# Optimization experiments

Hardware: AMD Instinct MI355X
Metric: run time of the kernel (lower is better)

## Reference

```python
import jax, jax.numpy as jnp
import numpy as np

B, T, C = 2, 2048, 1024
NHEADS = 16
HEAD_DIM = C // NHEADS  # 64
THETA = 10000.0
SCALE_BASE = 512.0
GN_EPS = 1e-5


def setup_inputs() -> dict:
    key = jax.random.key(0)
    ks = jax.random.split(key, 4)
    s = 0.02
    return {
        "x": jax.random.normal(ks[0], (B, T, C), jnp.float32),
        "w_qkv": jax.random.normal(ks[1], (3 * C, C), jnp.float32) * s,
        "w_gated": jax.random.normal(ks[2], (C, C), jnp.float32) * s,
        "w_proj": jax.random.normal(ks[3], (C, C), jnp.float32) * s,
        "gn_weight": jnp.ones((C,), jnp.float32),
        "gn_bias": jnp.zeros((C,), jnp.float32),
    }


def _rotate_half(x):
    # pairs are adjacent/interleaved: (d r) with r=2
    x1 = x[..., 0::2]
    x2 = x[..., 1::2]
    return jnp.stack([-x2, x1], axis=-1).reshape(x.shape)


def _rope_xpos(q, k, T):
    # lucidrains rotary_embedding_torch with use_xpos=True
    d = q.shape[-1]
    half = jnp.arange(0, d, 2, dtype=jnp.float32)
    inv_freq = 1.0 / (THETA ** (half / d))
    t = jnp.arange(T, dtype=jnp.float32)
    freqs = t[:, None] * inv_freq[None, :]          # [T, d/2]
    freqs = jnp.repeat(freqs, 2, axis=-1)           # [T, d] interleaved
    scale_vec = (half + 0.4 * d) / (1.4 * d)        # [d/2]
    power = (t - T // 2) / SCALE_BASE               # [T]
    scale = scale_vec[None, :] ** power[:, None]    # [T, d/2]
    scale = jnp.repeat(scale, 2, axis=-1)           # [T, d]
    cos, sin = jnp.cos(freqs), jnp.sin(freqs)
    q = q * (cos * scale) + _rotate_half(q) * (sin * scale)
    k = k * (cos / scale) + _rotate_half(k) * (sin / scale)
    return q, k


def _decay_mask(T):
    # gamma_h = 1 - 2^(-5-h); mask[h,i,j] = gamma_h^(i-j) for i>=j else 0
    gamma = 1.0 - 2.0 ** (-5.0 - jnp.arange(NHEADS, dtype=jnp.float32))
    idx = jnp.arange(T)
    diff = idx[:, None] - idx[None, :]              # [T, T]
    causal = diff >= 0
    expn = jnp.where(causal, diff, 0).astype(jnp.float32)
    return jnp.where(causal[None], gamma[:, None, None] ** expn[None], 0.0)


def reference(x, w_qkv, w_gated, w_proj, gn_weight, gn_bias):
    Bx, Tx, Cx = x.shape
    qkv = x @ w_qkv.T                               # [B,T,3C]
    q, k, v = jnp.split(qkv, 3, axis=-1)
    def to_heads(u):
        return u.reshape(Bx, Tx, NHEADS, HEAD_DIM).transpose(0, 2, 1, 3)
    q, k, v = to_heads(q), to_heads(k), to_heads(v)  # [B,H,T,D]
    q, k = _rope_xpos(q, k, Tx)
    mask = _decay_mask(Tx)                           # [H,T,T]
    scores = jnp.einsum('bhtd,bhsd->bhts', q, k) * (HEAD_DIM ** -0.5)
    scores = scores * mask[None]
    y = jnp.einsum('bhts,bhsd->bhtd', scores, v)     # [B,H,T,D]
    y = y.transpose(0, 2, 1, 3).reshape(Bx, Tx, Cx)  # [B,T,C]
    # GroupNorm over (B, C, T) with num_groups = NHEADS: normalize each
    # group's (C/H channels x T positions) jointly.
    yt = y.transpose(0, 2, 1).reshape(Bx, NHEADS, HEAD_DIM, Tx)
    mean = yt.mean(axis=(2, 3), keepdims=True)
    var = yt.var(axis=(2, 3), keepdims=True)
    yn = (yt - mean) / jnp.sqrt(var + GN_EPS)
    yn = yn.reshape(Bx, Cx, Tx)
    yn = yn * gn_weight[None, :, None] + gn_bias[None, :, None]
    yn = yn.transpose(0, 2, 1)                       # [B,T,C]
    out = jax.nn.silu(x @ w_gated.T) * yn
    return out @ w_proj.T
```

## Files before the change

kernel.cpp:

```cpp
#include <hip/hip_runtime.h>

typedef __attribute__((ext_vector_type(8))) short bf16x8;
typedef __attribute__((ext_vector_type(4))) float f32x4;
typedef __attribute__((ext_vector_type(16))) float f32x16;
typedef __attribute__((ext_vector_type(2))) unsigned short u16x2;
typedef __attribute__((ext_vector_type(4))) unsigned short u16x4;
typedef __attribute__((ext_vector_type(2))) unsigned int u32x2;

static constexpr int kB = 2;
static constexpr int kT = 2048;
static constexpr int kC = 1024;
static constexpr int kH = 16;
static constexpr int kD = 64;
static constexpr int kNC = 16;

__device__ inline unsigned short f2bf(float f) {
    unsigned int u = __float_as_uint(f);
    u += 0x7FFFu + ((u >> 16) & 1u);
    return (unsigned short)(u >> 16);
}
__device__ inline float bf2f(unsigned short u) {
    return __uint_as_float(((unsigned int)u) << 16);
}

#define GLDS16(g, s)                                                            \
    __builtin_amdgcn_global_load_lds(                                           \
        (const __attribute__((address_space(1))) unsigned int*)(g),             \
        (__attribute__((address_space(3))) unsigned int*)(s), 16, 0, 0)

__global__ __launch_bounds__(256) void cvt_bf16(const float* __restrict__ in,
                                                unsigned short* __restrict__ out, int n) {
    int i = (blockIdx.x * 256 + threadIdx.x) * 4;
    if (i >= n) return;
    float4 v = *(const float4*)(in + i);
    u16x4 o;
    o[0] = f2bf(v.x); o[1] = f2bf(v.y); o[2] = f2bf(v.z); o[3] = f2bf(v.w);
    *(u16x4*)(out + i) = o;
}

__global__ __launch_bounds__(256) void make_tables(float2* __restrict__ qtab,
                                                   float2* __restrict__ ktab,
                                                   float* __restrict__ decq,
                                                   float* __restrict__ deck) {
    int idx = blockIdx.x * 256 + threadIdx.x;
    if (idx < kT * 32) {
        int t = idx >> 5, i = idx & 31;
        float half = 2.0f * (float)i;
        float inv_freq = powf(10000.0f, -half / 64.0f);
        float fr = (float)t * inv_freq;
        float sv = (half + 0.4f * 64.0f) / (1.4f * 64.0f);
        float p = ((float)t - 1024.0f) / 512.0f;
        float scl = powf(sv, p);
        float c = cosf(fr), s = sinf(fr);
        qtab[idx] = make_float2(c * scl, s * scl);
        ktab[idx] = make_float2(c / scl, s / scl);
    }
    if (idx < kH * 128) {
        int h = idx >> 7, tt = idx & 127;
        float log2g = log2f(1.0f - exp2f(-5.0f - (float)h));
        decq[idx] = 0.125f * exp2f(log2g * (float)tt);
        deck[idx] = exp2f(-log2g * (float)tt);
    }
}

__global__ __launch_bounds__(256) void gemm_qkvg(const unsigned short* __restrict__ A,
                                                 const unsigned short* __restrict__ Bm,
                                                 unsigned short* __restrict__ qb,
                                                 unsigned short* __restrict__ kbuf,
                                                 unsigned short* __restrict__ vtb,
                                                 unsigned short* __restrict__ gbuf) {
    constexpr int K = 1024;
    __shared__ __align__(16) unsigned short Al[128 * 64];
    __shared__ __align__(16) unsigned short Bl[128 * 64];
    char* ab = (char*)Al;
    char* bb = (char*)Bl;
    const int tid = threadIdx.x;
    const int l = tid & 63, w = tid >> 6;
    const int wr = w >> 1, wc = w & 1;
    const int tm = blockIdx.y * 128, tn = blockIdx.x * 128;
    const int ri = l >> 3;
    const int su = (l & 7) ^ (ri & 7);

    f32x4 zero4 = {0.0f, 0.0f, 0.0f, 0.0f};
    f32x4 acc[4][4];
#pragma unroll
    for (int m = 0; m < 4; m++)
#pragma unroll
        for (int n = 0; n < 4; n++) acc[m][n] = zero4;

    for (int kt = 0; kt < K; kt += 64) {
#pragma unroll
        for (int c = w; c < 32; c += 4) {
            if (c < 16) {
                const unsigned short* src = A + (size_t)(tm + c * 8 + ri) * K + kt + su * 8;
                GLDS16(src, ab + c * 1024);
            } else {
                int cb = c - 16;
                const unsigned short* src = Bm + (size_t)(tn + cb * 8 + ri) * K + kt + su * 8;
                GLDS16(src, bb + cb * 1024);
            }
        }
        __syncthreads();
#pragma unroll
        for (int ks = 0; ks < 2; ks++) {
            bf16x8 af[4], bfr[4];
            int kbyte = ks * 64 + (l >> 4) * 16;
#pragma unroll
            for (int m = 0; m < 4; m++) {
                int row = wr * 64 + m * 16 + (l & 15);
                af[m] = *(const bf16x8*)(ab + row * 128 + (kbyte ^ ((row & 7) << 4)));
            }
#pragma unroll
            for (int n = 0; n < 4; n++) {
                int row = wc * 64 + n * 16 + (l & 15);
                bfr[n] = *(const bf16x8*)(bb + row * 128 + (kbyte ^ ((row & 7) << 4)));
            }
#pragma unroll
            for (int m = 0; m < 4; m++)
#pragma unroll
                for (int n = 0; n < 4; n++)
                    acc[m][n] = __builtin_amdgcn_mfma_f32_16x16x32_bf16(af[m], bfr[n], acc[m][n], 0, 0, 0);
        }
        __syncthreads();
    }

    if (tn < 2048) {
        const bool isq = (tn < 1024);
        unsigned short* dst = isq ? qb : kbuf;
        const int colbase = isq ? tn : (tn - 1024);
#pragma unroll
        for (int n = 0; n < 4; n++) {
            int col = colbase + wc * 64 + n * 16 + (l & 15);
            int h = col >> 6;
            int d = col & 63;
#pragma unroll
            for (int m = 0; m < 4; m++) {
#pragma unroll
                for (int r = 0; r < 4; r++) {
                    int row = tm + wr * 64 + m * 16 + (l >> 4) * 4 + r;
                    int b = row >> 11, t = row & 2047;
                    unsigned int ub = f2bf(acc[m][n][r]);
                    unsigned int pb = (unsigned int)__shfl_xor((int)ub, 1);
                    if (!(l & 1)) {
                        unsigned int packed = (ub & 0xFFFFu) | (pb << 16);
                        *(unsigned int*)(dst + ((size_t)(b * 16 + h) * 2048 + t) * 64 + d) = packed;
                    }
                }
            }
        }
    } else if (tn < 3072) {
#pragma unroll
        for (int m = 0; m < 4; m++)
#pragma unroll
            for (int n = 0; n < 4; n++) {
                int col2 = (tn - 2048) + wc * 64 + n * 16 + (l & 15);
                int rowb = tm + wr * 64 + m * 16 + (l >> 4) * 4;
                int b = rowb >> 11, t = rowb & 2047;
                u16x4 o;
#pragma unroll
                for (int r = 0; r < 4; r++) o[r] = f2bf(acc[m][n][r]);
                *(u16x4*)(vtb + ((size_t)(b * 1024 + col2)) * 2048 + t) = o;
            }
    } else {
#pragma unroll
        for (int n = 0; n < 4; n++) {
            int col3 = (tn - 3072) + wc * 64 + n * 16 + (l & 15);
#pragma unroll
            for (int m = 0; m < 4; m++) {
#pragma unroll
                for (int r = 0; r < 4; r++) {
                    int row = tm + wr * 64 + m * 16 + (l >> 4) * 4 + r;
                    float v = acc[m][n][r];
                    float sv2 = v / (1.0f + expf(-v));
                    unsigned int ub = f2bf(sv2);
                    unsigned int pb = (unsigned int)__shfl_xor((int)ub, 1);
                    if (!(l & 1)) {
                        unsigned int packed = (ub & 0xFFFFu) | (pb << 16);
                        *(unsigned int*)(gbuf + (size_t)row * 1024 + col3) = packed;
                    }
                }
            }
        }
    }
}

__global__ __launch_bounds__(256) void rope_qkt(unsigned short* __restrict__ qb,
                                                unsigned short* __restrict__ kbuf,
                                                unsigned short* __restrict__ ktb,
                                                const float2* __restrict__ qtab,
                                                const float2* __restrict__ ktab,
                                                const float* __restrict__ decq,
                                                const float* __restrict__ deck) {
    __shared__ unsigned short tile[64][72];
    const int bh = blockIdx.x;
    const int tt = blockIdx.y * 64;
    const int h = bh & 15;
    const int tl = threadIdx.x >> 2;
    const int du = (threadIdx.x & 3) * 16;
    const int t = tt + tl;
    const float dq = decq[h * 128 + (t & 127)];
    const float dk = deck[h * 128 + (t & 127)];

    {
        unsigned short* qrow = qb + ((size_t)bh * kT + t) * kD + du;
        bf16x8 a0 = *(const bf16x8*)(qrow);
        bf16x8 a1 = *(const bf16x8*)(qrow + 8);
        bf16x8 o0, o1;
#pragma unroll
        for (int j = 0; j < 4; ++j) {
            float2 cs = qtab[t * 32 + (du >> 1) + j];
            float x0 = bf2f((unsigned short)a0[2 * j]);
            float x1 = bf2f((unsigned short)a0[2 * j + 1]);
            o0[2 * j] = (short)f2bf((x0 * cs.x - x1 * cs.y) * dq);
            o0[2 * j + 1] = (short)f2bf((x1 * cs.x + x0 * cs.y) * dq);
            float2 cs2 = qtab[t * 32 + (du >> 1) + 4 + j];
            float y0 = bf2f((unsigned short)a1[2 * j]);
            float y1 = bf2f((unsigned short)a1[2 * j + 1]);
            o1[2 * j] = (short)f2bf((y0 * cs2.x - y1 * cs2.y) * dq);
            o1[2 * j + 1] = (short)f2bf((y1 * cs2.x + y0 * cs2.y) * dq);
        }
        *(bf16x8*)(qrow) = o0;
        *(bf16x8*)(qrow + 8) = o1;
    }
    {
        unsigned short* krow = kbuf + ((size_t)bh * kT + t) * kD + du;
        bf16x8 a0 = *(const bf16x8*)(krow);
        bf16x8 a1 = *(const bf16x8*)(krow + 8);
        bf16x8 o0, o1;
#pragma unroll
        for (int j = 0; j < 4; ++j) {
            float2 cs = ktab[t * 32 + (du >> 1) + j];
            float x0 = bf2f((unsigned short)a0[2 * j]);
            float x1 = bf2f((unsigned short)a0[2 * j + 1]);
            o0[2 * j] = (short)f2bf((x0 * cs.x - x1 * cs.y) * dk);
            o0[2 * j + 1] = (short)f2bf((x1 * cs.x + x0 * cs.y) * dk);
            float2 cs2 = ktab[t * 32 + (du >> 1) + 4 + j];
            float y0 = bf2f((unsigned short)a1[2 * j]);
            float y1 = bf2f((unsigned short)a1[2 * j + 1]);
            o1[2 * j] = (short)f2bf((y0 * cs2.x - y1 * cs2.y) * dk);
            o1[2 * j + 1] = (short)f2bf((y1 * cs2.x + y0 * cs2.y) * dk);
        }
        *(bf16x8*)(krow) = o0;
        *(bf16x8*)(krow + 8) = o1;
#pragma unroll
        for (int e = 0; e < 8; ++e) {
            tile[tl][du + e] = (unsigned short)o0[e];
            tile[tl][du + 8 + e] = (unsigned short)o1[e];
        }
    }
    __syncthreads();
    {
        int dd = threadIdx.x >> 2;
        int tb2 = (threadIdx.x & 3) * 16;
        bf16x8 o0, o1;
#pragma unroll
        for (int e = 0; e < 8; ++e) {
            o0[e] = (short)tile[tb2 + e][dd];
            o1[e] = (short)tile[tb2 + 8 + e][dd];
        }
        unsigned short* drow = ktb + ((size_t)bh * kD + dd) * kT + tt + tb2;
        *(bf16x8*)(drow) = o0;
        *(bf16x8*)(drow + 8) = o1;
    }
}

__global__ __launch_bounds__(256) void chunk_m(const unsigned short* __restrict__ ktb,
                                               const unsigned short* __restrict__ vtb,
                                               unsigned short* __restrict__ Mt) {
    __shared__ __align__(16) unsigned short Ktl[64 * 128];
    __shared__ __align__(16) unsigned short Vtl[64 * 128];
    const int tid = threadIdx.x, l = tid & 63, w = tid >> 6;
    const int bh = blockIdx.x, c = blockIdx.y, h = bh & 15;
    const int ql = l & 31, hi5 = l >> 5;
    char* kp = (char*)Ktl;
    char* vp = (char*)Vtl;
#pragma unroll
    for (int j = 0; j < 4; ++j) {
        int ch = w * 4 + j;
        int row = ch * 4 + (l >> 4);
        int u = (l & 15) ^ (row & 15);
        GLDS16(ktb + ((size_t)bh * kD + row) * kT + c * 128 + u * 8, kp + ch * 1024);
        GLDS16(vtb + ((size_t)bh * kD + row) * kT + c * 128 + u * 8, vp + ch * 1024);
    }
    __syncthreads();
    const int iw = w >> 1, jw = w & 1;
    f32x16 acc;
#pragma unroll
    for (int r = 0; r < 16; ++r) acc[r] = 0.0f;
#pragma unroll
    for (int sk = 0; sk < 8; ++sk) {
        int rowa = iw * 32 + ql;
        int rowb = jw * 32 + ql;
        bf16x8 av = *(const bf16x8*)(vp + rowa * 256 + 16 * ((2 * sk + hi5) ^ (rowa & 15)));
        bf16x8 bk = *(const bf16x8*)(kp + rowb * 256 + 16 * ((2 * sk + hi5) ^ (rowb & 15)));
        acc = __builtin_amdgcn_mfma_f32_32x32x16_bf16(av, bk, acc, 0, 0, 0);
    }
    float log2g = log2f(1.0f - exp2f(-5.0f - (float)h));
    float gC = exp2f(128.0f * log2g);
    unsigned short* mo = Mt + ((size_t)(bh * kNC + c)) * 4096;
#pragma unroll
    for (int r = 0; r < 16; ++r) {
        int row = iw * 32 + (r & 3) + 8 * (r >> 2) + 4 * hi5;
        int col = jw * 32 + ql;
        mo[row * 64 + col] = f2bf(acc[r] * gC);
    }
}

__global__ __launch_bounds__(256) void chunk_states(const unsigned short* __restrict__ Mt,
                                                    unsigned short* __restrict__ St) {
    const int bh = blockIdx.x, h = bh & 15;
    const int tid = threadIdx.x;
    float log2g = log2f(1.0f - exp2f(-5.0f - (float)h));
    float gC = exp2f(128.0f * log2g);
    float state[16];
#pragma unroll
    for (int e = 0; e < 16; ++e) state[e] = 0.0f;
    for (int c = 0; c < kNC; ++c) {
        unsigned short* so = St + ((size_t)(bh * kNC + c)) * 4096;
        const unsigned short* m = Mt + ((size_t)(bh * kNC + c)) * 4096;
#pragma unroll
        for (int k = 0; k < 4; ++k) {
            u16x4 o;
#pragma unroll
            for (int e = 0; e < 4; ++e) o[e] = f2bf(state[k * 4 + e]);
            *(u16x4*)(so + (k * 256 + tid) * 4) = o;
            u16x4 v = *(const u16x4*)(m + (k * 256 + tid) * 4);
#pragma unroll
            for (int e = 0; e < 4; ++e)
                state[k * 4 + e] = state[k * 4 + e] * gC + bf2f(v[e]);
        }
    }
}

__global__ __launch_bounds__(512) void chunk_attn(const unsigned short* __restrict__ qb,
                                                  const unsigned short* __restrict__ kb,
                                                  const unsigned short* __restrict__ vtb,
                                                  const unsigned short* __restrict__ St,
                                                  unsigned short* __restrict__ yb,
                                                  float* __restrict__ part) {
    __shared__ __align__(16) unsigned short Kt[128 * 64];
    __shared__ __align__(16) unsigned short Vt[64 * 128];
    __shared__ __align__(16) unsigned short Ss[64 * 64];
    __shared__ __align__(16) unsigned short Pl[8 * 32 * 64];
    __shared__ float red[16];
    const int tid = threadIdx.x, l = tid & 63, w = tid >> 6;
    const int bh = blockIdx.x, c = blockIdx.y;
    const int qw = w >> 1, dw = w & 1;
    const int ql = l & 31, hi5 = l >> 5;
    char* kp = (char*)Kt;
    char* vp = (char*)Vt;
    char* sp = (char*)Ss;
    char* pw = (char*)Pl + w * 4096;

#pragma unroll
    for (int j = 0; j < 2; ++j) {
        int ch = w * 2 + j;
        int row = ch * 8 + (l >> 3);
        int u = (l & 7) ^ (row & 7);
        GLDS16(kb + ((size_t)bh * kT + c * 128 + row) * kD + u * 8, kp + ch * 1024);
    }
#pragma unroll
    for (int j = 0; j < 2; ++j) {
        int ch = w * 2 + j;
        int row = ch * 4 + (l >> 4);
        int u = (l & 15) ^ (row & 15);
        GLDS16(vtb + ((size_t)bh * kD + row) * kT + c * 128 + u * 8, vp + ch * 1024);
    }
    {
        int row = w * 8 + (l >> 3);
        int u = (l & 7) ^ (row & 7);
        GLDS16(St + ((size_t)(bh * kNC + c)) * 4096 + row * 64 + u * 8, sp + w * 1024);
    }
    bf16x8 aq[4];
    {
        const unsigned short* qrow = qb + ((size_t)bh * kT + c * 128 + qw * 32 + ql) * kD + hi5 * 8;
#pragma unroll
        for (int dk = 0; dk < 4; ++dk) aq[dk] = *(const bf16x8*)(qrow + dk * 16);
    }
    __syncthreads();

    f32x16 acc;
#pragma unroll
    for (int r = 0; r < 16; ++r) acc[r] = 0.0f;
    const int qidx = qw * 32 + ql;

#pragma unroll
    for (int p = 0; p < 2; ++p) {
        f32x16 sA, sB;
#pragma unroll
        for (int r = 0; r < 16; ++r) { sA[r] = 0.0f; sB[r] = 0.0f; }
#pragma unroll
        for (int dk = 0; dk < 4; ++dk) {
            int rowa = (2 * p) * 32 + ql;
            int rowb = (2 * p + 1) * 32 + ql;
            bf16x8 ka = *(const bf16x8*)(kp + rowa * 128 + 16 * ((2 * dk + hi5) ^ (rowa & 7)));
            bf16x8 kb2 = *(const bf16x8*)(kp + rowb * 128 + 16 * ((2 * dk + hi5) ^ (rowb & 7)));
            sA = __builtin_amdgcn_mfma_f32_32x32x16_bf16(ka, aq[dk], sA, 0, 0, 0);
            sB = __builtin_amdgcn_mfma_f32_32x32x16_bf16(kb2, aq[dk], sB, 0, 0, 0);
        }
#pragma unroll
        for (int sb2 = 0; sb2 < 2; ++sb2) {
            int sbase = (2 * p + sb2) * 32 + 4 * hi5;
#pragma unroll
            for (int m = 0; m < 4; ++m) {
                float v0, v1, v2, v3;
                {
                    int s0i = sbase + 8 * m;
                    float x0 = sb2 ? sB[4 * m + 0] : sA[4 * m + 0];
                    float x1 = sb2 ? sB[4 * m + 1] : sA[4 * m + 1];
                    float x2 = sb2 ? sB[4 * m + 2] : sA[4 * m + 2];
                    float x3 = sb2 ? sB[4 * m + 3] : sA[4 * m + 3];
                    v0 = (qidx >= s0i + 0) ? x0 : 0.0f;
                    v1 = (qidx >= s0i + 1) ? x1 : 0.0f;
                    v2 = (qidx >= s0i + 2) ? x2 : 0.0f;
                    v3 = (qidx >= s0i + 3) ? x3 : 0.0f;
                }
                unsigned int lo, hi;
                asm("v_cvt_pk_bf16_f32 %0, %1, %2" : "=v"(lo) : "v"(v0), "v"(v1));
                asm("v_cvt_pk_bf16_f32 %0, %1, %2" : "=v"(hi) : "v"(v2), "v"(v3));
                u32x2 pr; pr[0] = lo; pr[1] = hi;
                *(u32x2*)(pw + ql * 128 + (((sb2 * 4 + m) * 16) ^ ((ql & 7) << 4)) + hi5 * 8) = pr;
            }
        }
#pragma unroll
        for (int kki = 0; kki < 4; ++kki) {
            bf16x8 ap = *(const bf16x8*)(pw + ql * 128 + 16 * ((2 * kki + hi5) ^ (ql & 7)));
            int rowv = dw * 32 + ql;
            bf16x8 bv = *(const bf16x8*)(vp + rowv * 256 + 16 * ((2 * (4 * p + kki) + hi5) ^ (rowv & 15)));
            acc = __builtin_amdgcn_mfma_f32_32x32x16_bf16(ap, bv, acc, 0, 0, 0);
        }
    }
#pragma unroll
    for (int dk = 0; dk < 4; ++dk) {
        int rows = dw * 32 + ql;
        bf16x8 bs = *(const bf16x8*)(sp + rows * 128 + 16 * ((2 * dk + hi5) ^ (rows & 7)));
        acc = __builtin_amdgcn_mfma_f32_32x32x16_bf16(aq[dk], bs, acc, 0, 0, 0);
    }
    float s = 0.0f, s2 = 0.0f;
#pragma unroll
    for (int r = 0; r < 16; ++r) {
        int row = c * 128 + qw * 32 + (r & 3) + 8 * (r >> 2) + 4 * hi5;
        int col = dw * 32 + ql;
        unsigned short ub = f2bf(acc[r]);
        yb[((size_t)bh * kT + row) * kD + col] = ub;
        float f = bf2f(ub);
        s += f; s2 += f * f;
    }
#pragma unroll
    for (int o = 32; o > 0; o >>= 1) {
        s += __shfl_down(s, o);
        s2 += __shfl_down(s2, o);
    }
    if (l == 0) { red[w * 2] = s; red[w * 2 + 1] = s2; }
    __syncthreads();
    if (tid == 0) {
        float S = 0.0f, S2 = 0.0f;
#pragma unroll
        for (int i = 0; i < 8; i++) { S += red[2 * i]; S2 += red[2 * i + 1]; }
        part[((size_t)bh * kNC + c) * 2] = S;
        part[((size_t)bh * kNC + c) * 2 + 1] = S2;
    }
}

__global__ __launch_bounds__(64) void gn_fin(const float* __restrict__ part,
                                             float* __restrict__ stats) {
    int bh = threadIdx.x;
    if (bh >= kB * kH) return;
    float S = 0.0f, S2 = 0.0f;
#pragma unroll
    for (int i = 0; i < kNC; i++) {
        S += part[(bh * kNC + i) * 2];
        S2 += part[(bh * kNC + i) * 2 + 1];
    }
    const float inv = 1.0f / (float)(kT * kD);
    float mean = S * inv;
    float var = S2 * inv - mean * mean;
    stats[2 * bh] = mean;
    stats[2 * bh + 1] = rsqrtf(var + 1e-5f);
}

__global__ __launch_bounds__(256) void gemm_proj(const unsigned short* __restrict__ A,
                                                 const unsigned short* __restrict__ Bm,
                                                 float* __restrict__ Cf,
                                                 int N, int K) {
    __shared__ __align__(16) unsigned short Al[128 * 64];
    __shared__ __align__(16) unsigned short Bl[128 * 64];
    char* ab = (char*)Al;
    char* bb = (char*)Bl;
    const int tid = threadIdx.x;
    const int l = tid & 63, w = tid >> 6;
    const int wr = w >> 1, wc = w & 1;
    const int tm = blockIdx.y * 128, tn = blockIdx.x * 128;
    const int ri = l >> 3;
    const int su = (l & 7) ^ (ri & 7);

    f32x4 zero4 = {0.0f, 0.0f, 0.0f, 0.0f};
    f32x4 acc[4][4];
#pragma unroll
    for (int m = 0; m < 4; m++)
#pragma unroll
        for (int n = 0; n < 4; n++) acc[m][n] = zero4;

    for (int kt = 0; kt < K; kt += 64) {
#pragma unroll
        for (int c = w; c < 32; c += 4) {
            if (c < 16) {
                const unsigned short* src = A + (size_t)(tm + c * 8 + ri) * K + kt + su * 8;
                GLDS16(src, ab + c * 1024);
            } else {
                int cb = c - 16;
                const unsigned short* src = Bm + (size_t)(tn + cb * 8 + ri) * K + kt + su * 8;
                GLDS16(src, bb + cb * 1024);
            }
        }
        __syncthreads();
#pragma unroll
        for (int ks = 0; ks < 2; ks++) {
            bf16x8 af[4], bfr[4];
            int kbyte = ks * 64 + (l >> 4) * 16;
#pragma unroll
            for (int m = 0; m < 4; m++) {
                int row = wr * 64 + m * 16 + (l & 15);
                af[m] = *(const bf16x8*)(ab + row * 128 + (kbyte ^ ((row & 7) << 4)));
            }
#pragma unroll
            for (int n = 0; n < 4; n++) {
                int row = wc * 64 + n * 16 + (l & 15);
                bfr[n] = *(const bf16x8*)(bb + row * 128 + (kbyte ^ ((row & 7) << 4)));
            }
#pragma unroll
            for (int m = 0; m < 4; m++)
#pragma unroll
                for (int n = 0; n < 4; n++)
                    acc[m][n] = __builtin_amdgcn_mfma_f32_16x16x32_bf16(af[m], bfr[n], acc[m][n], 0, 0, 0);
        }
        __syncthreads();
    }
#pragma unroll
    for (int m = 0; m < 4; m++)
#pragma unroll
        for (int n = 0; n < 4; n++)
#pragma unroll
            for (int r = 0; r < 4; r++) {
                int row = tm + wr * 64 + m * 16 + (l >> 4) * 4 + r;
                int col = tn + wc * 64 + n * 16 + (l & 15);
                Cf[(size_t)row * N + col] = acc[m][n][r];
            }
}

__global__ __launch_bounds__(256) void fuse_z(const unsigned short* __restrict__ gb,
                                              const unsigned short* __restrict__ yb,
                                              const float* __restrict__ stats,
                                              const float* __restrict__ gnw,
                                              const float* __restrict__ gnb,
                                              unsigned short* __restrict__ z) {
    int idx = blockIdx.x * 256 + threadIdx.x;
    int row = idx >> 8;
    int c = (idx & 255) << 2;
    int b = row >> 11, t = row & 2047;
    int h = c >> 6, d = c & 63;
    int bh = b * kH + h;
    u16x4 gv = *(const u16x4*)(gb + (size_t)row * kC + c);
    u16x4 yv = *(const u16x4*)(yb + (((size_t)bh * kT) + t) * kD + d);
    float mean = stats[2 * bh], rstd = stats[2 * bh + 1];
    float4 wv = *(const float4*)(gnw + c);
    float4 bv = *(const float4*)(gnb + c);
    u16x4 o;
    o[0] = f2bf(bf2f(gv[0]) * ((bf2f(yv[0]) - mean) * rstd * wv.x + bv.x));
    o[1] = f2bf(bf2f(gv[1]) * ((bf2f(yv[1]) - mean) * rstd * wv.y + bv.y));
    o[2] = f2bf(bf2f(gv[2]) * ((bf2f(yv[2]) - mean) * rstd * wv.z + bv.z));
    o[3] = f2bf(bf2f(gv[3]) * ((bf2f(yv[3]) - mean) * rstd * wv.w + bv.w));
    *(u16x4*)(z + (size_t)row * kC + c) = o;
}

extern "C" void kernel_launch(void* const* d_in, const int* in_sizes, int n_in,
                              void* d_out, int out_size, void* d_ws, size_t ws_size,
                              hipStream_t stream) {
    const float* x = (const float*)d_in[0];
    const float* w_qkv = (const float*)d_in[1];
    const float* w_gated = (const float*)d_in[2];
    const float* w_proj = (const float*)d_in[3];
    const float* gnw = (const float*)d_in[4];
    const float* gnb = (const float*)d_in[5];
    float* out = (float*)d_out;
    char* ws = (char*)d_ws;

    unsigned short* xb      = (unsigned short*)(ws + 0);
    unsigned short* wqkvb   = (unsigned short*)(ws + 8388608);
    unsigned short* wgatedb = (unsigned short*)(ws + 14680064);
    unsigned short* wprojb  = (unsigned short*)(ws + 16777216);
    unsigned short* qb      = (unsigned short*)(ws + 18874368);
    unsigned short* kbuf    = (unsigned short*)(ws + 27262976);
    unsigned short* vtb     = (unsigned short*)(ws + 35651584);
    unsigned short* zb      = (unsigned short*)(ws + 44040192);
    float* part  = (float*)(ws + 44040192);
    float* stats = (float*)(ws + 52428800);
    float2* qtab = (float2*)(ws + 52429056);
    float2* ktab = (float2*)(ws + 52953344);
    float*  decq = (float*)(ws + 53477632);
    float*  deck = (float*)(ws + 53485824);
    unsigned short* Mt  = (unsigned short*)(ws + 52429056);
    unsigned short* St  = (unsigned short*)(ws + 56623360);
    unsigned short* yb  = (unsigned short*)(ws + 60817664);
    unsigned short* gbuf= (unsigned short*)(ws + 69206272);
    unsigned short* ktb = (unsigned short*)(ws + 77594880);

    cvt_bf16<<<4096, 256, 0, stream>>>(x, xb, kB * kT * kC);
    cvt_bf16<<<3072, 256, 0, stream>>>(w_qkv, wqkvb, 3 * kC * kC);
    cvt_bf16<<<1024, 256, 0, stream>>>(w_gated, wgatedb, kC * kC);
    cvt_bf16<<<1024, 256, 0, stream>>>(w_proj, wprojb, kC * kC);
    make_tables<<<256, 256, 0, stream>>>(qtab, ktab, decq, deck);

    gemm_qkvg<<<dim3(32, 32), 256, 0, stream>>>(xb, wqkvb, qb, kbuf, vtb, gbuf);

    rope_qkt<<<dim3(kB * kH, kT / 64), 256, 0, stream>>>(qb, kbuf, ktb, qtab, ktab, decq, deck);

    chunk_m<<<dim3(kB * kH, kNC), 256, 0, stream>>>(ktb, vtb, Mt);
    chunk_states<<<kB * kH, 256, 0, stream>>>(Mt, St);
    chunk_attn<<<dim3(kB * kH, kNC), 512, 0, stream>>>(qb, kbuf, vtb, St, yb, part);

    gn_fin<<<1, 64, 0, stream>>>(part, stats);

    fuse_z<<<4096, 256, 0, stream>>>(gbuf, yb, stats, gnw, gnb, zb);

    gemm_proj<<<dim3(kC / 128, 4096 / 128), 256, 0, stream>>>(zb, wprojb, out, kC, kC);
}
```

Baseline: 139.0 us.

## Merge bf16 conversions into one launch, shrink proj GEMM tile, simplify gate store

```diff
diff --git a/kernel.cpp b/kernel.cpp
--- a/kernel.cpp
+++ b/kernel.cpp
@@ -28,11 +28,20 @@
         (const __attribute__((address_space(1))) unsigned int*)(g),             \
         (__attribute__((address_space(3))) unsigned int*)(s), 16, 0, 0)
 
-__global__ __launch_bounds__(256) void cvt_bf16(const float* __restrict__ in,
-                                                unsigned short* __restrict__ out, int n) {
+__global__ __launch_bounds__(256) void cvt_all(const float* __restrict__ x,
+                                               const float* __restrict__ wq,
+                                               const float* __restrict__ wg,
+                                               const float* __restrict__ wp,
+                                               unsigned short* __restrict__ out) {
     int i = (blockIdx.x * 256 + threadIdx.x) * 4;
-    if (i >= n) return;
-    float4 v = *(const float4*)(in + i);
+    if (i >= 9437184) return;
+    const float* src;
+    int rel;
+    if (i < 4194304) { src = x;  rel = i; }
+    else if (i < 7340032) { src = wq; rel = i - 4194304; }
+    else if (i < 8388608) { src = wg; rel = i - 7340032; }
+    else { src = wp; rel = i - 8388608; }
+    float4 v = *(const float4*)(src + rel);
     u16x4 o;
     o[0] = f2bf(v.x); o[1] = f2bf(v.y); o[2] = f2bf(v.z); o[3] = f2bf(v.w);
     *(u16x4*)(out + i) = o;
@@ -163,24 +172,17 @@
             }
     } else {
 #pragma unroll
-        for (int n = 0; n < 4; n++) {
-            int col3 = (tn - 3072) + wc * 64 + n * 16 + (l & 15);
-#pragma unroll
-            for (int m = 0; m < 4; m++) {
+        for (int m = 0; m < 4; m++)
+#pragma unroll
+            for (int n = 0; n < 4; n++)
 #pragma unroll
                 for (int r = 0; r < 4; r++) {
                     int row = tm + wr * 64 + m * 16 + (l >> 4) * 4 + r;
+                    int col3 = (tn - 3072) + wc * 64 + n * 16 + (l & 15);
                     float v = acc[m][n][r];
                     float sv2 = v / (1.0f + expf(-v));
-                    unsigned int ub = f2bf(sv2);
-                    unsigned int pb = (unsigned int)__shfl_xor((int)ub, 1);
-                    if (!(l & 1)) {
-                        unsigned int packed = (ub & 0xFFFFu) | (pb << 16);
-                        *(unsigned int*)(gbuf + (size_t)row * 1024 + col3) = packed;
-                    }
+                    gbuf[(size_t)row * 1024 + col3] = f2bf(sv2);
                 }
-            }
-        }
     }
 }
 
@@ -484,26 +486,26 @@
                                                  float* __restrict__ Cf,
                                                  int N, int K) {
     __shared__ __align__(16) unsigned short Al[128 * 64];
-    __shared__ __align__(16) unsigned short Bl[128 * 64];
+    __shared__ __align__(16) unsigned short Bl[64 * 64];
     char* ab = (char*)Al;
     char* bb = (char*)Bl;
     const int tid = threadIdx.x;
     const int l = tid & 63, w = tid >> 6;
     const int wr = w >> 1, wc = w & 1;
-    const int tm = blockIdx.y * 128, tn = blockIdx.x * 128;
+    const int tm = blockIdx.y * 128, tn = blockIdx.x * 64;
     const int ri = l >> 3;
     const int su = (l & 7) ^ (ri & 7);
 
     f32x4 zero4 = {0.0f, 0.0f, 0.0f, 0.0f};
-    f32x4 acc[4][4];
+    f32x4 acc[4][2];
 #pragma unroll
     for (int m = 0; m < 4; m++)
 #pragma unroll
-        for (int n = 0; n < 4; n++) acc[m][n] = zero4;
+        for (int n = 0; n < 2; n++) acc[m][n] = zero4;
 
     for (int kt = 0; kt < K; kt += 64) {
 #pragma unroll
-        for (int c = w; c < 32; c += 4) {
+        for (int c = w; c < 24; c += 4) {
             if (c < 16) {
                 const unsigned short* src = A + (size_t)(tm + c * 8 + ri) * K + kt + su * 8;
                 GLDS16(src, ab + c * 1024);
@@ -516,7 +518,7 @@
         __syncthreads();
 #pragma unroll
         for (int ks = 0; ks < 2; ks++) {
-            bf16x8 af[4], bfr[4];
+            bf16x8 af[4], bfr[2];
             int kbyte = ks * 64 + (l >> 4) * 16;
 #pragma unroll
             for (int m = 0; m < 4; m++) {
@@ -524,14 +526,14 @@
                 af[m] = *(const bf16x8*)(ab + row * 128 + (kbyte ^ ((row & 7) << 4)));
             }
 #pragma unroll
-            for (int n = 0; n < 4; n++) {
-                int row = wc * 64 + n * 16 + (l & 15);
+            for (int n = 0; n < 2; n++) {
+                int row = wc * 32 + n * 16 + (l & 15);
                 bfr[n] = *(const bf16x8*)(bb + row * 128 + (kbyte ^ ((row & 7) << 4)));
             }
 #pragma unroll
             for (int m = 0; m < 4; m++)
 #pragma unroll
-                for (int n = 0; n < 4; n++)
+                for (int n = 0; n < 2; n++)
                     acc[m][n] = __builtin_amdgcn_mfma_f32_16x16x32_bf16(af[m], bfr[n], acc[m][n], 0, 0, 0);
         }
         __syncthreads();
@@ -539,11 +541,11 @@
 #pragma unroll
     for (int m = 0; m < 4; m++)
 #pragma unroll
-        for (int n = 0; n < 4; n++)
+        for (int n = 0; n < 2; n++)
 #pragma unroll
             for (int r = 0; r < 4; r++) {
                 int row = tm + wr * 64 + m * 16 + (l >> 4) * 4 + r;
-                int col = tn + wc * 64 + n * 16 + (l & 15);
+                int col = tn + wc * 32 + n * 16 + (l & 15);
                 Cf[(size_t)row * N + col] = acc[m][n][r];
             }
 }
@@ -587,7 +589,6 @@
 
     unsigned short* xb      = (unsigned short*)(ws + 0);
     unsigned short* wqkvb   = (unsigned short*)(ws + 8388608);
-    unsigned short* wgatedb = (unsigned short*)(ws + 14680064);
     unsigned short* wprojb  = (unsigned short*)(ws + 16777216);
     unsigned short* qb      = (unsigned short*)(ws + 18874368);
     unsigned short* kbuf    = (unsigned short*)(ws + 27262976);
@@ -605,10 +606,7 @@
     unsigned short* gbuf= (unsigned short*)(ws + 69206272);
     unsigned short* ktb = (unsigned short*)(ws + 77594880);
 
-    cvt_bf16<<<4096, 256, 0, stream>>>(x, xb, kB * kT * kC);
-    cvt_bf16<<<3072, 256, 0, stream>>>(w_qkv, wqkvb, 3 * kC * kC);
-    cvt_bf16<<<1024, 256, 0, stream>>>(w_gated, wgatedb, kC * kC);
-    cvt_bf16<<<1024, 256, 0, stream>>>(w_proj, wprojb, kC * kC);
+    cvt_all<<<9216, 256, 0, stream>>>(x, w_qkv, w_gated, w_proj, xb);
     make_tables<<<256, 256, 0, stream>>>(qtab, ktab, decq, deck);
 
     gemm_qkvg<<<dim3(32, 32), 256, 0, stream>>>(xb, wqkvb, qb, kbuf, vtb, gbuf);
@@ -623,5 +621,5 @@
 
     fuse_z<<<4096, 256, 0, stream>>>(gbuf, yb, stats, gnw, gnb, zb);
 
-    gemm_proj<<<dim3(kC / 128, 4096 / 128), 256, 0, stream>>>(zb, wprojb, out, kC, kC);
-}
+    gemm_proj<<<dim3(kC / 64, 4096 / 128), 256, 0, stream>>>(zb, wprojb, out, kC, kC);
+}
```

New measurement: 123.2 us. -11.4%, faster.
